# Kernel tuning notes

Hardware: AMD Instinct MI355X
Metric: run time of the kernel (lower is better)

The kernel has to match this reference:

```python
import jax, jax.numpy as jnp
import numpy as np

EPS = 1e-10
FAR_DELTA = 1e10  # matches torch code's 10000000000.0 sentinel last delta


def setup_inputs() -> dict:
    key = jax.random.key(0)
    k1, k2, k3 = jax.random.split(key, 3)
    N, D, C = 65536, 128, 3
    # nonnegative densities, as produced by a NeRF density head
    density = jax.random.uniform(k1, (N, D), dtype=jnp.float32) * 2.0
    feature = jax.random.uniform(k2, (N, D, C), dtype=jnp.float32)
    # depth samples must be increasing along the sample dim (near=2.0, far=6.0)
    depth_values = jnp.sort(
        2.0 + 4.0 * jax.random.uniform(k3, (N, D), dtype=jnp.float32), axis=-1
    )
    return {"density": density, "feature": feature, "depth_values": depth_values}


def reference(density, feature, depth_values):
    # deltas: consecutive depth diffs, last delta = 1e10 (as in the torch code)
    deltas = jnp.concatenate(
        [depth_values[:, 1:] - depth_values[:, :-1],
         jnp.full_like(depth_values[:, :1], FAR_DELTA)],
        axis=-1,
    )  # (N, d)
    # log per-segment transmittance term: exp(-sigma*delta + eps) per original
    s = -density * deltas + EPS  # (N, d)
    # exclusive cumulative product via exclusive cumsum in log space
    log_T = jnp.concatenate(
        [jnp.zeros_like(s[:, :1]), jnp.cumsum(s[:, :-1], axis=1)], axis=1
    )
    T = jnp.exp(log_T)  # (N, d) transmittance
    weights = T * (1.0 - jnp.exp(s))  # (N, d)
    feat = jnp.einsum("nd,ndc->nc", weights, feature)  # (N, C)
    depth = jnp.sum(weights * depth_values, axis=1)  # (N,)
    return feat, depth
```

## Files before the change

### kernel.cpp

```cpp
#include <hip/hip_runtime.h>
#include <math.h>

#define EPS 1e-10f
#define FAR_DELTA 1e10f

__global__ void __launch_bounds__(256) volrend_d128(
    const float* __restrict__ density,
    const float* __restrict__ feature,
    const float* __restrict__ depth,
    float* __restrict__ out_feat,
    float* __restrict__ out_depth,
    int N)
{
    const int half = threadIdx.x >> 5;
    const int rlane = threadIdx.x & 31;
    const int ray = blockIdx.x * 8 + half;
    if (ray >= N) return;

    const float4 dp = *reinterpret_cast<const float4*>(depth   + (size_t)ray * 128 + 4 * rlane);
    const float4 dn = *reinterpret_cast<const float4*>(density + (size_t)ray * 128 + 4 * rlane);
    const float4* fp = reinterpret_cast<const float4*>(feature + (size_t)ray * 384 + 12 * rlane);
    const float4 fA = fp[0];
    const float4 fB = fp[1];
    const float4 fC = fp[2];

    const float dnext = __shfl_down(dp.x, 1, 32);
    const float delta0 = dp.y - dp.x;
    const float delta1 = dp.z - dp.y;
    const float delta2 = dp.w - dp.z;
    const float delta3 = (rlane == 31) ? FAR_DELTA : (dnext - dp.w);

    const float s0 = fmaf(-dn.x, delta0, EPS);
    const float s1 = fmaf(-dn.y, delta1, EPS);
    const float s2 = fmaf(-dn.z, delta2, EPS);
    const float s3 = fmaf(-dn.w, delta3, EPS);

    const float s3_scan = (rlane == 31) ? 0.0f : s3;
    const float quad = s0 + s1 + s2 + s3_scan;
    float scan = quad;
    #pragma unroll
    for (int off = 1; off < 32; off <<= 1) {
        const float t = __shfl_up(scan, off, 32);
        if (rlane >= off) scan += t;
    }
    const float excl = scan - quad;
    const float logT0 = excl;
    const float logT1 = excl + s0;
    const float logT2 = logT1 + s1;
    const float logT3 = logT2 + s2;

    const float w0 = __expf(logT0) * (1.0f - __expf(s0));
    const float w1 = __expf(logT1) * (1.0f - __expf(s1));
    const float w2 = __expf(logT2) * (1.0f - __expf(s2));
    const float w3 = __expf(logT3) * (1.0f - __expf(s3));

    float fa0 = w0 * fA.x + w1 * fA.w + w2 * fB.z + w3 * fC.y;
    float fa1 = w0 * fA.y + w1 * fB.x + w2 * fB.w + w3 * fC.z;
    float fa2 = w0 * fA.z + w1 * fB.y + w2 * fC.x + w3 * fC.w;
    float da  = w0 * dp.x + w1 * dp.y + w2 * dp.z + w3 * dp.w;

    #pragma unroll
    for (int off = 16; off >= 1; off >>= 1) {
        fa0 += __shfl_xor(fa0, off);
        fa1 += __shfl_xor(fa1, off);
        fa2 += __shfl_xor(fa2, off);
        da  += __shfl_xor(da,  off);
    }

    if (rlane == 0) {
        out_feat[(size_t)ray * 3 + 0] = fa0;
        out_feat[(size_t)ray * 3 + 1] = fa1;
        out_feat[(size_t)ray * 3 + 2] = fa2;
        out_depth[ray] = da;
    }
}

__global__ void volrend_generic(
    const float* __restrict__ density,
    const float* __restrict__ feature,
    const float* __restrict__ depth,
    float* __restrict__ out,
    int N, int D, int C)
{
    const int ray = blockIdx.x * blockDim.x + threadIdx.x;
    if (ray >= N) return;
    float logT = 0.0f;
    float facc[8];
    for (int c = 0; c < 8; ++c) facc[c] = 0.0f;
    float dacc = 0.0f;
    const size_t base = (size_t)ray * D;
    for (int d = 0; d < D; ++d) {
        const float dv = depth[base + d];
        const float delta = (d == D - 1) ? FAR_DELTA : (depth[base + d + 1] - dv);
        const float s = fmaf(-density[base + d], delta, EPS);
        const float w = expf(logT) * (1.0f - expf(s));
        for (int c = 0; c < C && c < 8; ++c)
            facc[c] += w * feature[(base + d) * C + c];
        dacc += w * dv;
        logT += s;
    }
    for (int c = 0; c < C && c < 8; ++c) out[(size_t)ray * C + c] = facc[c];
    out[(size_t)N * C + ray] = dacc;
}

extern "C" void kernel_launch(void* const* d_in, const int* in_sizes, int n_in,
                              void* d_out, int out_size, void* d_ws, size_t ws_size,
                              hipStream_t stream) {
    const float* density = (const float*)d_in[0];
    const float* feature = (const float*)d_in[1];
    const float* depth   = (const float*)d_in[2];
    float* out = (float*)d_out;

    const long ND  = in_sizes[0];
    const long NDC = in_sizes[1];
    const int C = (int)(NDC / ND);
    const int N = out_size / (C + 1);
    const int D = (int)(ND / N);

    if (D == 128 && C == 3) {
        const int blocks = (N + 7) / 8;
        volrend_d128<<<blocks, 256, 0, stream>>>(density, feature, depth,
                                                 out, out + (size_t)N * 3, N);
    } else {
        const int threads = 256;
        volrend_generic<<<(N + threads - 1) / threads, threads, 0, stream>>>(
            density, feature, depth, out, N, D, C);
    }
}
```

Measured before the change: 29.35 us.

## Use persistent grid-stride loop with software prefetch of next ray

Converts the one-ray-per-32-lane-group kernel into a persistent grid-stride loop capped at 2048 blocks. Each group prefetches the next ray's depth, density and feature vectors into registers while it computes the current ray. The aim is to overlap memory latency with compute and cut block launch overhead. In exchange it raises register pressure and lowers the number of blocks in flight, which can reduce memory-level parallelism on a bandwidth-bound kernel.

```diff
diff --git a/kernel.cpp b/kernel.cpp
--- a/kernel.cpp
+++ b/kernel.cpp
@@ -12,66 +12,87 @@
     float* __restrict__ out_depth,
     int N)
 {
-    const int half = threadIdx.x >> 5;
     const int rlane = threadIdx.x & 31;
-    const int ray = blockIdx.x * 8 + half;
+    const int group = (blockIdx.x * blockDim.x + threadIdx.x) >> 5;
+    const int gstride = (gridDim.x * blockDim.x) >> 5;
+
+    int ray = group;
     if (ray >= N) return;
 
-    const float4 dp = *reinterpret_cast<const float4*>(depth   + (size_t)ray * 128 + 4 * rlane);
-    const float4 dn = *reinterpret_cast<const float4*>(density + (size_t)ray * 128 + 4 * rlane);
-    const float4* fp = reinterpret_cast<const float4*>(feature + (size_t)ray * 384 + 12 * rlane);
-    const float4 fA = fp[0];
-    const float4 fB = fp[1];
-    const float4 fC = fp[2];
+    float4 dp = *reinterpret_cast<const float4*>(depth   + (size_t)ray * 128 + 4 * rlane);
+    float4 dn = *reinterpret_cast<const float4*>(density + (size_t)ray * 128 + 4 * rlane);
+    const float4* fp0 = reinterpret_cast<const float4*>(feature + (size_t)ray * 384 + 12 * rlane);
+    float4 fA = fp0[0];
+    float4 fB = fp0[1];
+    float4 fC = fp0[2];
 
-    const float dnext = __shfl_down(dp.x, 1, 32);
-    const float delta0 = dp.y - dp.x;
-    const float delta1 = dp.z - dp.y;
-    const float delta2 = dp.w - dp.z;
-    const float delta3 = (rlane == 31) ? FAR_DELTA : (dnext - dp.w);
+    while (true) {
+        const int nray = ray + gstride;
+        const bool have_next = nray < N;
 
-    const float s0 = fmaf(-dn.x, delta0, EPS);
-    const float s1 = fmaf(-dn.y, delta1, EPS);
-    const float s2 = fmaf(-dn.z, delta2, EPS);
-    const float s3 = fmaf(-dn.w, delta3, EPS);
+        float4 ndp, ndn, nfA, nfB, nfC;
+        if (have_next) {
+            ndp = *reinterpret_cast<const float4*>(depth   + (size_t)nray * 128 + 4 * rlane);
+            ndn = *reinterpret_cast<const float4*>(density + (size_t)nray * 128 + 4 * rlane);
+            const float4* nfp = reinterpret_cast<const float4*>(feature + (size_t)nray * 384 + 12 * rlane);
+            nfA = nfp[0];
+            nfB = nfp[1];
+            nfC = nfp[2];
+        }
 
-    const float s3_scan = (rlane == 31) ? 0.0f : s3;
-    const float quad = s0 + s1 + s2 + s3_scan;
-    float scan = quad;
-    #pragma unroll
-    for (int off = 1; off < 32; off <<= 1) {
-        const float t = __shfl_up(scan, off, 32);
-        if (rlane >= off) scan += t;
-    }
-    const float excl = scan - quad;
-    const float logT0 = excl;
-    const float logT1 = excl + s0;
-    const float logT2 = logT1 + s1;
-    const float logT3 = logT2 + s2;
+        const float dnext = __shfl_down(dp.x, 1, 32);
+        const float delta0 = dp.y - dp.x;
+        const float delta1 = dp.z - dp.y;
+        const float delta2 = dp.w - dp.z;
+        const float delta3 = (rlane == 31) ? FAR_DELTA : (dnext - dp.w);
 
-    const float w0 = __expf(logT0) * (1.0f - __expf(s0));
-    const float w1 = __expf(logT1) * (1.0f - __expf(s1));
-    const float w2 = __expf(logT2) * (1.0f - __expf(s2));
-    const float w3 = __expf(logT3) * (1.0f - __expf(s3));
+        const float s0 = fmaf(-dn.x, delta0, EPS);
+        const float s1 = fmaf(-dn.y, delta1, EPS);
+        const float s2 = fmaf(-dn.z, delta2, EPS);
+        const float s3 = fmaf(-dn.w, delta3, EPS);
 
-    float fa0 = w0 * fA.x + w1 * fA.w + w2 * fB.z + w3 * fC.y;
-    float fa1 = w0 * fA.y + w1 * fB.x + w2 * fB.w + w3 * fC.z;
-    float fa2 = w0 * fA.z + w1 * fB.y + w2 * fC.x + w3 * fC.w;
-    float da  = w0 * dp.x + w1 * dp.y + w2 * dp.z + w3 * dp.w;
+        const float s3_scan = (rlane == 31) ? 0.0f : s3;
+        const float quad = s0 + s1 + s2 + s3_scan;
+        float scan = quad;
+        #pragma unroll
+        for (int off = 1; off < 32; off <<= 1) {
+            const float t = __shfl_up(scan, off, 32);
+            if (rlane >= off) scan += t;
+        }
+        const float excl = scan - quad;
+        const float logT0 = excl;
+        const float logT1 = excl + s0;
+        const float logT2 = logT1 + s1;
+        const float logT3 = logT2 + s2;
 
-    #pragma unroll
-    for (int off = 16; off >= 1; off >>= 1) {
-        fa0 += __shfl_xor(fa0, off);
-        fa1 += __shfl_xor(fa1, off);
-        fa2 += __shfl_xor(fa2, off);
-        da  += __shfl_xor(da,  off);
-    }
+        const float w0 = __expf(logT0) * (1.0f - __expf(s0));
+        const float w1 = __expf(logT1) * (1.0f - __expf(s1));
+        const float w2 = __expf(logT2) * (1.0f - __expf(s2));
+        const float w3 = __expf(logT3) * (1.0f - __expf(s3));
 
-    if (rlane == 0) {
-        out_feat[(size_t)ray * 3 + 0] = fa0;
-        out_feat[(size_t)ray * 3 + 1] = fa1;
-        out_feat[(size_t)ray * 3 + 2] = fa2;
-        out_depth[ray] = da;
+        float fa0 = w0 * fA.x + w1 * fA.w + w2 * fB.z + w3 * fC.y;
+        float fa1 = w0 * fA.y + w1 * fB.x + w2 * fB.w + w3 * fC.z;
+        float fa2 = w0 * fA.z + w1 * fB.y + w2 * fC.x + w3 * fC.w;
+        float da  = w0 * dp.x + w1 * dp.y + w2 * dp.z + w3 * dp.w;
+
+        #pragma unroll
+        for (int off = 16; off >= 1; off >>= 1) {
+            fa0 += __shfl_xor(fa0, off);
+            fa1 += __shfl_xor(fa1, off);
+            fa2 += __shfl_xor(fa2, off);
+            da  += __shfl_xor(da,  off);
+        }
+
+        if (rlane == 0) {
+            out_feat[(size_t)ray * 3 + 0] = fa0;
+            out_feat[(size_t)ray * 3 + 1] = fa1;
+            out_feat[(size_t)ray * 3 + 2] = fa2;
+            out_depth[ray] = da;
+        }
+
+        if (!have_next) break;
+        ray = nray;
+        dp = ndp; dn = ndn; fA = nfA; fB = nfB; fC = nfC;
     }
 }
 
@@ -118,7 +139,9 @@
     const int D = (int)(ND / N);
 
     if (D == 128 && C == 3) {
-        const int blocks = (N + 7) / 8;
+        int groups_needed = (N + 0);
+        int blocks = 2048;
+        if (blocks * 8 > groups_needed) blocks = (groups_needed + 7) / 8;
         volrend_d128<<<blocks, 256, 0, stream>>>(density, feature, depth,
                                                  out, out + (size_t)N * 3, N);
     } else {
```

After: 31.38 us. 1.07x slower.
